# Kernel tuning notes

Measured on AMD Instinct MI355X. Metric: run time of the kernel, lower is better.

Reference implementation:

```python
import jax, jax.numpy as jnp
import numpy as np

B, N, D, H, HID = 8, 729, 1152, 12, 4304
HD = D // H
EPS = 1e-6


def _layer_norm(x, g, b):
    mu = jnp.mean(x, axis=-1, keepdims=True)
    var = jnp.mean((x - mu) ** 2, axis=-1, keepdims=True)
    return (x - mu) / jnp.sqrt(var + EPS) * g + b


def setup_inputs() -> dict:
    key = jax.random.key(0)
    ks = jax.random.split(key, 9)
    s = 0.02
    return {
        "x": jax.random.normal(ks[0], (B, N, D), jnp.float32),
        "wq": jax.random.normal(ks[1], (D, D), jnp.float32) * s,
        "bq": jnp.zeros((D,), jnp.float32),
        "wk": jax.random.normal(ks[2], (D, D), jnp.float32) * s,
        "bk": jnp.zeros((D,), jnp.float32),
        "wv": jax.random.normal(ks[3], (D, D), jnp.float32) * s,
        "bv": jnp.zeros((D,), jnp.float32),
        "wo": jax.random.normal(ks[4], (D, D), jnp.float32) * s,
        "bo": jnp.zeros((D,), jnp.float32),
        "ln1_g": jnp.ones((D,), jnp.float32),
        "ln1_b": jnp.zeros((D,), jnp.float32),
        "w_fc1": jax.random.normal(ks[5], (HID, D), jnp.float32) * s,
        "b_fc1": jnp.zeros((HID,), jnp.float32),
        "w_fc2": jax.random.normal(ks[6], (D, HID), jnp.float32) * s,
        "b_fc2": jnp.zeros((D,), jnp.float32),
        "ln2_g": jnp.ones((D,), jnp.float32),
        "ln2_b": jnp.zeros((D,), jnp.float32),
    }


def reference(x, wq, bq, wk, bk, wv, bv, wo, bo, ln1_g, ln1_b,
              w_fc1, b_fc1, w_fc2, b_fc2, ln2_g, ln2_b):
    b, n, d = x.shape
    # split_heads in the source is a plain view (B, H, N, HD) -- NOT a transpose.
    def heads(t):
        return t.reshape(b, H, n, HD)

    Q = heads(x @ wq.T + bq)
    K = heads(x @ wk.T + bk)
    V = heads(x @ wv.T + bv)

    scores = jnp.einsum("bhqd,bhkd->bhqk", Q, K) * (HD ** -0.5)
    attn_w = jax.nn.softmax(scores, axis=-1)
    o = jnp.einsum("bhqk,bhkd->bhqd", attn_w, V)  # [B,H,N,HD]
    o = jnp.swapaxes(o, 1, 2).reshape(b, n, d)
    attn_out = o @ wo.T + bo

    # post-norm: LN(sublayer) + residual
    h = _layer_norm(attn_out, ln1_g, ln1_b) + x

    # quirky MLP: activation applied BEFORE fc1 (faithful to source)
    m = jax.nn.gelu(h, approximate=True)
    m = m @ w_fc1.T + b_fc1
    m = m @ w_fc2.T + b_fc2

    return _layer_norm(m, ln2_g, ln2_b) + h
```

## Files before the change

### kernel.cpp

```cpp
#include <hip/hip_runtime.h>
#include <hip/hip_bf16.h>

#define BF16 __hip_bfloat16

typedef short short8 __attribute__((ext_vector_type(8)));
typedef short short4v __attribute__((ext_vector_type(4)));
typedef float v4f __attribute__((ext_vector_type(4)));
typedef float f4 __attribute__((ext_vector_type(4)));

__device__ float g_bp[1152];

__device__ __forceinline__ short f2bs(float f) {
    __hip_bfloat16 h = __float2bfloat16(f);
    return *(short*)&h;
}

__device__ __forceinline__ float bs2f(short s) {
    __hip_bfloat16 h = *(__hip_bfloat16*)&s;
    return __bfloat162float(h);
}

__device__ __forceinline__ void async_cp16(const BF16* g, BF16* l) {
    __builtin_amdgcn_global_load_lds(
        (const __attribute__((address_space(1))) void*)g,
        (__attribute__((address_space(3))) void*)l,
        16, 0, 0);
}

__global__ __launch_bounds__(256) void prep_kernel(
    const float* __restrict__ wq, const float* __restrict__ wk,
    const float* __restrict__ wv, const float* __restrict__ wo,
    const float* __restrict__ wfc1, const float* __restrict__ wfc2,
    const float* __restrict__ x,
    const float* __restrict__ bfc1, const float* __restrict__ bfc2,
    BF16* __restrict__ wbq, BF16* __restrict__ wbk,
    BF16* __restrict__ wbv, BF16* __restrict__ wbo,
    BF16* __restrict__ wbf1t, BF16* __restrict__ wbf2,
    BF16* __restrict__ xb)
{
    __shared__ float tile[64][65];
    const int bid = blockIdx.x;
    const int tid = threadIdx.x;

    if (bid < 16641) {
        const int i = bid * 256 + tid;
        constexpr int N_DD  = 331776;
        constexpr int N4    = 4 * N_DD;
        constexpr int N_F2  = 1253376;
        constexpr int E_F2  = N4 + N_F2;
        constexpr int N_X   = 1679616;
        constexpr int TOTAL = E_F2 + N_X;

        if (i < N4) {
            int seg = i / N_DD, j = i - seg * N_DD;
            const float* s = (seg == 0) ? wq : (seg == 1) ? wk : (seg == 2) ? wv : wo;
            BF16* d = (seg == 0) ? wbq : (seg == 1) ? wbk : (seg == 2) ? wbv : wbo;
            f4 v = ((const f4*)s)[j];
            short4v o = {f2bs(v.x), f2bs(v.y), f2bs(v.z), f2bs(v.w)};
            ((short4v*)d)[j] = o;
        } else if (i < E_F2) {
            int j = i - N4;
            int row = j / 1088;
            int c = (j - row * 1088) * 4;
            short4v o = {0, 0, 0, 0};
            if (c < 4304) {
                f4 v = *(const f4*)(wfc2 + (size_t)row * 4304 + c);
                o[0] = f2bs(v.x); o[1] = f2bs(v.y); o[2] = f2bs(v.z); o[3] = f2bs(v.w);
            }
            *(short4v*)(wbf2 + (size_t)row * 4352 + c) = o;
        } else if (i < TOTAL) {
            int j = i - E_F2;
            f4 v = ((const f4*)x)[j];
            short4v o = {f2bs(v.x), f2bs(v.y), f2bs(v.z), f2bs(v.w)};
            ((short4v*)xb)[j] = o;
        }
    } else if (bid < 17865) {
        const int b2 = bid - 16641;
        const int h0 = (b2 % 68) * 64;
        const int d0 = (b2 / 68) * 64;
#pragma unroll
        for (int i = 0; i < 4; ++i) {
            int lin = tid + i * 256;
            int r = lin >> 4, c4 = lin & 15;
            f4 v = {0.f, 0.f, 0.f, 0.f};
            if (h0 + r < 4304)
                v = *(const f4*)(wfc1 + (size_t)(h0 + r) * 1152 + d0 + c4 * 4);
            tile[r][c4 * 4 + 0] = v.x;
            tile[r][c4 * 4 + 1] = v.y;
            tile[r][c4 * 4 + 2] = v.z;
            tile[r][c4 * 4 + 3] = v.w;
        }
        __syncthreads();
#pragma unroll
        for (int i = 0; i < 2; ++i) {
            int lin = tid + i * 256;
            int dr = lin >> 3, h8 = lin & 7;
            short8 o;
#pragma unroll
            for (int e = 0; e < 8; ++e)
                o[e] = f2bs(tile[h8 * 8 + e][dr]);
            *(short8*)(wbf1t + (size_t)(d0 + dr) * 4352 + h0 + h8 * 8) = o;
        }
    } else {
        const int row = (bid - 17865) * 4 + (tid >> 6);
        const int lane = tid & 63;
        const float* wr = wfc2 + (size_t)row * 4304;
        float s = 0.f;
        for (int k = lane; k < 4304; k += 64) s += wr[k] * bfc1[k];
#pragma unroll
        for (int mm = 1; mm < 64; mm <<= 1) s += __shfl_xor(s, mm, 64);
        if (lane == 0) g_bp[row] = s + bfc2[row];
    }
}

__global__ __launch_bounds__(256) void qkv_merge_kernel(
    const BF16* __restrict__ A,
    const BF16* __restrict__ Wqkv,
    const float* __restrict__ b0, const float* __restrict__ b1,
    const float* __restrict__ b2,
    BF16* __restrict__ C, size_t cstride, int M,
    const BF16* __restrict__ W2,
    const BF16* __restrict__ W1t,
    float* __restrict__ P)
{
    __shared__ __align__(16) BF16 smem[256 * 64];
    const int bid  = blockIdx.x;
    const int tid  = threadIdx.x;
    const int lane = tid & 63;
    const int wave = tid >> 6;
    const int quad = lane >> 4;
    const int l16  = lane & 15;
    const v4f zf = {0.f, 0.f, 0.f, 0.f};

    if (bid < 324) {
        BF16* As = smem;
        BF16* Bs = smem + 64 * 64;
        const int mx = bid % 18, ny = (bid / 18) % 9, z = bid / 162;
        const int m0 = mx * 64, n0 = ny * 128;
        const int ks0 = z * 34;
        const int wm = (wave >> 1) * 32;
        const int wn = (wave & 1) * 64;

        v4f acc[2][4];
#pragma unroll
        for (int i = 0; i < 2; ++i)
#pragma unroll
            for (int j = 0; j < 4; ++j) acc[i][j] = zf;

        const BF16* gA[2]; BF16* lA[2];
#pragma unroll
        for (int i = 0; i < 2; ++i) {
            int c = tid + i * 256;
            gA[i] = W2 + (size_t)(m0 + (c >> 3)) * 4352 + ((((c & 7) - (c >> 3)) & 7) << 3)
                  + ks0 * 64;
            lA[i] = As + (c & ~63) * 8;
        }
        const BF16* gB[4]; BF16* lB[4];
#pragma unroll
        for (int i = 0; i < 4; ++i) {
            int c = tid + i * 256;
            gB[i] = W1t + (size_t)(n0 + (c >> 3)) * 4352 + ((((c & 7) - (c >> 3)) & 7) << 3)
                  + ks0 * 64;
            lB[i] = Bs + (c & ~63) * 8;
        }

        for (int kt = 0; kt < 34; ++kt) {
#pragma unroll
            for (int i = 0; i < 2; ++i) { async_cp16(gA[i], lA[i]); gA[i] += 64; }
#pragma unroll
            for (int i = 0; i < 4; ++i)  { async_cp16(gB[i], lB[i]); gB[i] += 64; }
            __syncthreads();
#pragma unroll
            for (int ks = 0; ks < 2; ++ks) {
                short8 af[2], bfg[4];
#pragma unroll
                for (int mt = 0; mt < 2; ++mt) {
                    int row = wm + mt * 16 + l16;
                    af[mt] = *(const short8*)(As + row * 64 + ((((ks << 2) | quad) + row & 7) & 7) * 8);
                }
#pragma unroll
                for (int nt = 0; nt < 4; ++nt) {
                    int row = wn + nt * 16 + l16;
                    bfg[nt] = *(const short8*)(Bs + row * 64 + ((((ks << 2) | quad) + row & 7) & 7) * 8);
                }
#pragma unroll
                for (int mt = 0; mt < 2; ++mt)
#pragma unroll
                    for (int nt = 0; nt < 4; ++nt)
                        acc[mt][nt] = __builtin_amdgcn_mfma_f32_16x16x32_bf16(
                            af[mt], bfg[nt], acc[mt][nt], 0, 0, 0);
            }
            __syncthreads();
        }

        float* Pz = P + (size_t)z * 1327104;
#pragma unroll
        for (int mt = 0; mt < 2; ++mt)
#pragma unroll
            for (int nt = 0; nt < 4; ++nt)
#pragma unroll
                for (int r2 = 0; r2 < 4; ++r2) {
                    int row = m0 + wm + mt * 16 + quad * 4 + r2;
                    int col = n0 + wn + nt * 16 + l16;
                    Pz[(size_t)row * 1152 + col] = acc[mt][nt][r2];
                }
    } else {
        BF16* As = smem;
        BF16* Bs = smem + 128 * 64;
        const int id2 = bid - 324;
        const int m0 = (id2 % 46) * 128;
        const int n0 = (id2 / 46) * 128;
        const int wm = (wave >> 1) * 64;
        const int wn = (wave & 1) * 64;

        v4f acc[4][4];
#pragma unroll
        for (int i = 0; i < 4; ++i)
#pragma unroll
            for (int j = 0; j < 4; ++j) acc[i][j] = zf;

        const BF16* gA[4]; BF16* lA[4];
        const BF16* gB[4]; BF16* lB[4];
#pragma unroll
        for (int i = 0; i < 4; ++i) {
            int c = tid + i * 256;
            int src = ((((c & 7) - (c >> 3)) & 7) << 3);
            gA[i] = A + (size_t)(m0 + (c >> 3)) * 1152 + src;
            gB[i] = Wqkv + (size_t)(n0 + (c >> 3)) * 1152 + src;
            lA[i] = As + (c & ~63) * 8;
            lB[i] = Bs + (c & ~63) * 8;
        }

        for (int kt = 0; kt < 18; ++kt) {
#pragma unroll
            for (int i = 0; i < 4; ++i) { async_cp16(gA[i], lA[i]); gA[i] += 64; }
#pragma unroll
            for (int i = 0; i < 4; ++i) { async_cp16(gB[i], lB[i]); gB[i] += 64; }
            __syncthreads();
#pragma unroll
            for (int ks = 0; ks < 2; ++ks) {
                short8 af[4], bfg[4];
#pragma unroll
                for (int mt = 0; mt < 4; ++mt) {
                    int row = wm + mt * 16 + l16;
                    af[mt] = *(const short8*)(As + row * 64 + ((((ks << 2) | quad) + row & 7) & 7) * 8);
                }
#pragma unroll
                for (int nt = 0; nt < 4; ++nt) {
                    int row = wn + nt * 16 + l16;
                    bfg[nt] = *(const short8*)(Bs + row * 64 + ((((ks << 2) | quad) + row & 7) & 7) * 8);
                }
#pragma unroll
                for (int mt = 0; mt < 4; ++mt)
#pragma unroll
                    for (int nt = 0; nt < 4; ++nt)
                        acc[mt][nt] = __builtin_amdgcn_mfma_f32_16x16x32_bf16(
                            af[mt], bfg[nt], acc[mt][nt], 0, 0, 0);
            }
            __syncthreads();
        }

        const int sel = n0 / 1152;
        const float* bp = (sel == 0) ? b0 : (sel == 1) ? b1 : b2;
        BF16* Cb = C + (size_t)sel * cstride;
        const int nl0 = n0 - sel * 1152;

        float bv[4];
#pragma unroll
        for (int nt = 0; nt < 4; ++nt)
            bv[nt] = bp[nl0 + wn + nt * 16 + l16];
#pragma unroll
        for (int mt = 0; mt < 4; ++mt)
#pragma unroll
            for (int nt = 0; nt < 4; ++nt)
#pragma unroll
                for (int r2 = 0; r2 < 4; ++r2) {
                    int row_l = wm + mt * 16 + quad * 4 + r2;
                    int col_l = wn + nt * 16 + l16;
                    smem[row_l * 128 + col_l] = __float2bfloat16(acc[mt][nt][r2] + bv[nt]);
                }
        __syncthreads();
#pragma unroll
        for (int p = 0; p < 8; ++p) {
            int idx = p * 256 + tid;
            int row = m0 + (idx >> 4);
            if (row < M)
                *(short8*)(Cb + (size_t)row * 1152 + nl0 + (idx & 15) * 8) =
                    *(const short8*)(smem + idx * 8);
        }
    }
}

__global__ __launch_bounds__(256) void trans_reduce_kernel(
    const BF16* __restrict__ V, BF16* __restrict__ VT,
    const float* __restrict__ P, BF16* __restrict__ Wm)
{
    __shared__ __align__(16) BF16 tl[64][128];
    const int bid = blockIdx.x, tid = threadIdx.x;
    const short8 zero8 = {0, 0, 0, 0, 0, 0, 0, 0};

    if (bid < 1152) {
        const int hg = bid / 12, kb = bid - hg * 12;
        const int b = hg / 12, hh = hg - b * 12;
        const BF16* src = V + (size_t)b * 839808 + (size_t)hh * 69984;
        BF16* dst = VT + (size_t)hg * 86016;
        const int kk0 = kb * 64;
#pragma unroll
        for (int i = 0; i < 3; ++i) {
            int c = tid + i * 256;
            int r = c / 12, cg = c - r * 12;
            short8 v = (kk0 + r < 729)
                ? *(const short8*)(src + (size_t)(kk0 + r) * 96 + cg * 8) : zero8;
            *(short8*)(&tl[r][(cg ^ ((r >> 3) & 7)) * 8]) = v;
        }
        __syncthreads();
#pragma unroll
        for (int i = 0; i < 3; ++i) {
            int wc = tid + i * 256;
            int hd = wc >> 3, o = wc & 7;
            int sp = (((hd >> 3) ^ o) << 3) + (hd & 7);
            short8 out;
#pragma unroll
            for (int j = 0; j < 8; ++j)
                out[j] = *(const short*)&tl[o * 8 + j][sp];
            *(short8*)(dst + (size_t)hd * 768 + kk0 + o * 8) = out;
        }
    } else if (bid < 1728) {
        int c = (bid - 1152) * 256 + tid;
        int hg = c / 1536, rem = c - hg * 1536;
        int r = rem / 96, ock = rem - r * 96;
        int kk = ock * 8;
        short8 v = zero8;
        if (r == 0) {
            const short oneb = 0x3F80;
#pragma unroll
            for (int j = 0; j < 8; ++j) v[j] = (kk + j < 729) ? oneb : (short)0;
        }
        *(short8*)(VT + (size_t)hg * 86016 + (size_t)(96 + r) * 768 + kk) = v;
    } else {
        int i = (bid - 1728) * 256 + tid;
        f4 s = ((const f4*)P)[i];
        f4 v = ((const f4*)(P + 1327104))[i];
        s.x += v.x; s.y += v.y; s.z += v.z; s.w += v.w;
        short4v o = {f2bs(s.x), f2bs(s.y), f2bs(s.z), f2bs(s.w)};
        ((short4v*)Wm)[i] = o;
    }
}

template<int TM>
__global__ __launch_bounds__(256) void gemm_bt_t(
    const BF16* __restrict__ A, int lda,
    const BF16* __restrict__ W, int ldb,
    const float* __restrict__ bias, int nbias,
    BF16* __restrict__ C, int ldc,
    int M, int Kr)
{
    constexpr int MT = TM / 32;
    __shared__ __align__(16) BF16 smem[(TM + 128) * 64];
    BF16* As = smem;
    BF16* Bs = smem + TM * 64;

    const int tid  = threadIdx.x;
    const int lane = tid & 63;
    const int wave = tid >> 6;
    const int quad = lane >> 4;
    const int l16  = lane & 15;
    const int wm   = (wave >> 1) * (TM / 2);
    const int wn   = (wave & 1) * 64;
    const int m0   = blockIdx.x * TM;
    const int n0   = blockIdx.y * 128;
    if (m0 >= M) return;

    const v4f zf = {0.f, 0.f, 0.f, 0.f};
    v4f acc[MT][4];
#pragma unroll
    for (int i = 0; i < MT; ++i)
#pragma unroll
        for (int j = 0; j < 4; ++j) acc[i][j] = zf;

    const BF16* gA[MT]; BF16* lA[MT];
#pragma unroll
    for (int i = 0; i < MT; ++i) {
        int c = tid + i * 256;
        gA[i] = A + (size_t)(m0 + (c >> 3)) * lda + ((((c & 7) - (c >> 3)) & 7) << 3);
        lA[i] = As + (c & ~63) * 8;
    }
    const BF16* gB[4]; BF16* lB[4];
#pragma unroll
    for (int i = 0; i < 4; ++i) {
        int c = tid + i * 256;
        gB[i] = W + (size_t)(n0 + (c >> 3)) * ldb + ((((c & 7) - (c >> 3)) & 7) << 3);
        lB[i] = Bs + (c & ~63) * 8;
    }

    const int nk = Kr >> 6;
    for (int kt = 0; kt < nk; ++kt) {
#pragma unroll
        for (int i = 0; i < MT; ++i) { async_cp16(gA[i], lA[i]); gA[i] += 64; }
#pragma unroll
        for (int i = 0; i < 4; ++i)  { async_cp16(gB[i], lB[i]); gB[i] += 64; }
        __syncthreads();

#pragma unroll
        for (int ks = 0; ks < 2; ++ks) {
            short8 af[MT], bfg[4];
#pragma unroll
            for (int mt = 0; mt < MT; ++mt) {
                int row = wm + mt * 16 + l16;
                af[mt] = *(const short8*)(As + row * 64 + ((((ks << 2) | quad) + row & 7) & 7) * 8);
            }
#pragma unroll
            for (int nt = 0; nt < 4; ++nt) {
                int row = wn + nt * 16 + l16;
                bfg[nt] = *(const short8*)(Bs + row * 64 + ((((ks << 2) | quad) + row & 7) & 7) * 8);
            }
#pragma unroll
            for (int mt = 0; mt < MT; ++mt)
#pragma unroll
                for (int nt = 0; nt < 4; ++nt)
                    acc[mt][nt] = __builtin_amdgcn_mfma_f32_16x16x32_bf16(
                        af[mt], bfg[nt], acc[mt][nt], 0, 0, 0);
        }
        __syncthreads();
    }

    float bv[4];
#pragma unroll
    for (int nt = 0; nt < 4; ++nt) {
        int col = n0 + wn + nt * 16 + l16;
        bv[nt] = (col < nbias) ? bias[col] : 0.f;
    }
#pragma unroll
    for (int mt = 0; mt < MT; ++mt)
#pragma unroll
        for (int nt = 0; nt < 4; ++nt)
#pragma unroll
            for (int r2 = 0; r2 < 4; ++r2) {
                int row_l = wm + mt * 16 + quad * 4 + r2;
                int col_l = wn + nt * 16 + l16;
                smem[row_l * 128 + col_l] = __float2bfloat16(acc[mt][nt][r2] + bv[nt]);
            }
    __syncthreads();
#pragma unroll
    for (int p = 0; p < TM / 16; ++p) {
        int idx = p * 256 + tid;
        int row = m0 + (idx >> 4);
        if (row < M)
            *(short8*)(C + (size_t)row * ldc + n0 + (idx & 15) * 8) =
                *(const short8*)(smem + idx * 8);
    }
}

__global__ __launch_bounds__(256) void attn_flash3(
    const BF16* __restrict__ Q, const BF16* __restrict__ K,
    const BF16* __restrict__ VT, BF16* __restrict__ O)
{
    constexpr int NQ = 729, HDk = 96, DM = 1152, LDV = 768;
    __shared__ __align__(16) BF16 Ks[64 * 104];
    __shared__ __align__(16) BF16 Vs[112 * 64];
    __shared__ __align__(16) BF16 Ps[4][32 * 72];

    const int id = blockIdx.x;
    const int xcd = id & 7, slot = id >> 3;
    const int hb = slot / 6, qt = slot - hb * 6;
    const int hg = xcd * 12 + hb;
    const int b = hg / 12, hh = hg - b * 12;

    const int tid = threadIdx.x, wave = tid >> 6, lane = tid & 63;
    const int quad = lane >> 4, l16 = lane & 15;
    const size_t kbase = (size_t)b * (NQ * DM) + (size_t)hh * (NQ * HDk);
    const size_t vbase = (size_t)hg * 112 * LDV;

    const short8 zero8 = {0, 0, 0, 0, 0, 0, 0, 0};
    const v4f zf = {0.f, 0.f, 0.f, 0.f};
    const float C2 = 0.14724445f;

    const int q0w = qt * 128 + wave * 32;
    short8 aq[2][3];
#pragma unroll
    for (int mt = 0; mt < 2; ++mt) {
        int qrow = q0w + mt * 16 + l16;
#pragma unroll
        for (int ks = 0; ks < 3; ++ks)
            aq[mt][ks] = (qrow < NQ)
                ? *(const short8*)(Q + kbase + (size_t)qrow * HDk + ks * 32 + quad * 8)
                : zero8;
    }

    int kk_[3], kg_[3];
#pragma unroll
    for (int i = 0; i < 3; ++i) {
        int c = tid + i * 256;
        kk_[i] = c / 12; kg_[i] = c - kk_[i] * 12;
    }
    int vq_[4], vgr_[4], vhd_[4];
#pragma unroll
    for (int i = 0; i < 4; ++i) {
        int q = wave + 4 * i;
        vq_[i] = q;
        int hd = q * 8 + (lane >> 3);
        vhd_[i] = hd;
        vgr_[i] = ((lane & 7) - hd) & 7;
    }

    v4f oacc[2][7];
#pragma unroll
    for (int mt = 0; mt < 2; ++mt)
#pragma unroll
        for (int nt = 0; nt < 7; ++nt) oacc[mt][nt] = zf;

    for (int kt = 0; kt < 12; ++kt) {
        const int k0 = kt * 64;
#pragma unroll
        for (int i = 0; i < 4; ++i) {
            if (vq_[i] < 14)
                async_cp16(VT + vbase + (size_t)vhd_[i] * LDV + k0 + vgr_[i] * 8,
                           Vs + vq_[i] * 512);
        }
#pragma unroll
        for (int i = 0; i < 3; ++i) {
            short8 v = *(const short8*)(K + kbase + (size_t)(k0 + kk_[i]) * HDk + kg_[i] * 8);
            *(short8*)(Ks + kk_[i] * 104 + kg_[i] * 8) = v;
        }
        __syncthreads();

        v4f s[2][4];
#pragma unroll
        for (int mt = 0; mt < 2; ++mt)
#pragma unroll
            for (int nt = 0; nt < 4; ++nt) s[mt][nt] = zf;
#pragma unroll
        for (int ks = 0; ks < 3; ++ks)
#pragma unroll
            for (int nt = 0; nt < 4; ++nt) {
                short8 bk = *(const short8*)(Ks + (nt * 16 + l16) * 104 + ks * 32 + quad * 8);
#pragma unroll
                for (int mt = 0; mt < 2; ++mt)
                    s[mt][nt] = __builtin_amdgcn_mfma_f32_16x16x32_bf16(
                        aq[mt][ks], bk, s[mt][nt], 0, 0, 0);
            }

        BF16* Pw = &Ps[wave][0];
#pragma unroll
        for (int mt = 0; mt < 2; ++mt)
#pragma unroll
            for (int nt = 0; nt < 4; ++nt)
#pragma unroll
                for (int r = 0; r < 4; ++r)
                    Pw[(mt * 16 + quad * 4 + r) * 72 + nt * 16 + l16] =
                        __float2bfloat16(exp2f(s[mt][nt][r] * C2));
        asm volatile("s_waitcnt lgkmcnt(0)" ::: "memory");

        short8 ap[2][2];
#pragma unroll
        for (int mt = 0; mt < 2; ++mt)
#pragma unroll
            for (int kc = 0; kc < 2; ++kc)
                ap[mt][kc] = *(const short8*)(Pw + (mt * 16 + l16) * 72 + kc * 32 + quad * 8);
#pragma unroll
        for (int nt = 0; nt < 7; ++nt) {
            int hd = nt * 16 + l16;
#pragma unroll
            for (int kc = 0; kc < 2; ++kc) {
                short8 bv = *(const short8*)(Vs + hd * 64 + (((kc * 4 + quad) + hd & 7) & 7) * 8);
#pragma unroll
                for (int mt = 0; mt < 2; ++mt)
                    oacc[mt][nt] = __builtin_amdgcn_mfma_f32_16x16x32_bf16(
                        ap[mt][kc], bv, oacc[mt][nt], 0, 0, 0);
            }
        }
        __syncthreads();
    }

#pragma unroll
    for (int mt = 0; mt < 2; ++mt) {
        const int qb = q0w + mt * 16 + quad * 4;
#pragma unroll
        for (int r = 0; r < 4; ++r) {
            int q = qb + r;
            float lv = __shfl(oacc[mt][6][r], quad << 4, 64);
            float inv = (lv > 0.f) ? 1.f / lv : 0.f;
            if (q >= NQ) continue;
#pragma unroll
            for (int nt = 0; nt < 6; ++nt)
                O[(size_t)b * (NQ * DM) + (size_t)q * DM + hh * HDk + nt * 16 + l16] =
                    __float2bfloat16(oacc[mt][nt][r] * inv);
        }
    }
}

__device__ __forceinline__ float block_sum256(float v, float* red, int tid)
{
#pragma unroll
    for (int mm = 1; mm < 64; mm <<= 1) v += __shfl_xor(v, mm, 64);
    if ((tid & 63) == 0) red[tid >> 6] = v;
    __syncthreads();
    float r = red[0] + red[1] + red[2] + red[3];
    __syncthreads();
    return r;
}

__global__ __launch_bounds__(256) void ln1_gelu_kernel(
    const BF16* __restrict__ ao, const float* __restrict__ x,
    const float* __restrict__ gw, const float* __restrict__ bw,
    BF16* __restrict__ hout, BF16* __restrict__ gout)
{
    __shared__ float red[4];
    const int row = blockIdx.x, tid = threadIdx.x;
    const bool act = tid < 144;
    float v[8];
    float s = 0.f;
    if (act) {
        short8 pk = ((const short8*)(ao + (size_t)row * 1152))[tid];
#pragma unroll
        for (int j = 0; j < 8; ++j) { v[j] = bs2f(pk[j]); s += v[j]; }
    } else {
#pragma unroll
        for (int j = 0; j < 8; ++j) v[j] = 0.f;
    }
    s = block_sum256(s, red, tid);
    float mu = s * (1.f / 1152.f);
    float vsum = 0.f;
    if (act) {
#pragma unroll
        for (int j = 0; j < 8; ++j) { float d = v[j] - mu; vsum += d * d; }
    }
    vsum = block_sum256(vsum, red, tid);
    float rstd = rsqrtf(vsum * (1.f / 1152.f) + 1e-6f);
    if (act) {
        f4 g0 = ((const f4*)gw)[2 * tid], g1 = ((const f4*)gw)[2 * tid + 1];
        f4 b0 = ((const f4*)bw)[2 * tid], b1 = ((const f4*)bw)[2 * tid + 1];
        const f4* xr = (const f4*)(x + (size_t)row * 1152);
        f4 x0 = xr[2 * tid], x1 = xr[2 * tid + 1];
        short8 ho, go;
#pragma unroll
        for (int j = 0; j < 8; ++j) {
            float gj = (j < 4) ? g0[j] : g1[j - 4];
            float bj = (j < 4) ? b0[j] : b1[j - 4];
            float xj = (j < 4) ? x0[j] : x1[j - 4];
            float hv = (v[j] - mu) * rstd * gj + bj + xj;
            ho[j] = f2bs(hv);
            float t = hv;
            float gl = 0.5f * t * (1.f + tanhf(0.7978845608028654f * (t + 0.044715f * t * t * t)));
            go[j] = f2bs(gl);
        }
        ((short8*)(hout + (size_t)row * 1152))[tid] = ho;
        ((short8*)(gout + (size_t)row * 1152))[tid] = go;
    }
}

__global__ __launch_bounds__(256) void ln2_kernel(
    const BF16* __restrict__ m2, const BF16* __restrict__ hf,
    const float* __restrict__ gw, const float* __restrict__ bw,
    float* __restrict__ out)
{
    __shared__ float red[4];
    const int row = blockIdx.x, tid = threadIdx.x;
    const bool act = tid < 144;
    float v[8];
    float s = 0.f;
    if (act) {
        short8 pk = ((const short8*)(m2 + (size_t)row * 1152))[tid];
#pragma unroll
        for (int j = 0; j < 8; ++j) { v[j] = bs2f(pk[j]); s += v[j]; }
    } else {
#pragma unroll
        for (int j = 0; j < 8; ++j) v[j] = 0.f;
    }
    s = block_sum256(s, red, tid);
    float mu = s * (1.f / 1152.f);
    float vsum = 0.f;
    if (act) {
#pragma unroll
        for (int j = 0; j < 8; ++j) { float d = v[j] - mu; vsum += d * d; }
    }
    vsum = block_sum256(vsum, red, tid);
    float rstd = rsqrtf(vsum * (1.f / 1152.f) + 1e-6f);
    if (act) {
        f4 g0 = ((const f4*)gw)[2 * tid], g1 = ((const f4*)gw)[2 * tid + 1];
        f4 b0 = ((const f4*)bw)[2 * tid], b1 = ((const f4*)bw)[2 * tid + 1];
        short8 hfv = ((const short8*)(hf + (size_t)row * 1152))[tid];
        f4 o0, o1;
#pragma unroll
        for (int j = 0; j < 8; ++j) {
            float gj = (j < 4) ? g0[j] : g1[j - 4];
            float bj = (j < 4) ? b0[j] : b1[j - 4];
            float ov = (v[j] - mu) * rstd * gj + bj + bs2f(hfv[j]);
            if (j < 4) o0[j] = ov; else o1[j - 4] = ov;
        }
        f4* orow = (f4*)(out + (size_t)row * 1152);
        orow[2 * tid] = o0;
        orow[2 * tid + 1] = o1;
    }
}

extern "C" void kernel_launch(void* const* d_in, const int* in_sizes, int n_in,
                              void* d_out, int out_size, void* d_ws, size_t ws_size,
                              hipStream_t stream)
{
    const float* x    = (const float*)d_in[0];
    const float* wq   = (const float*)d_in[1];
    const float* bq   = (const float*)d_in[2];
    const float* wk   = (const float*)d_in[3];
    const float* bk   = (const float*)d_in[4];
    const float* wv   = (const float*)d_in[5];
    const float* bv   = (const float*)d_in[6];
    const float* wo   = (const float*)d_in[7];
    const float* bo   = (const float*)d_in[8];
    const float* ln1g = (const float*)d_in[9];
    const float* ln1b = (const float*)d_in[10];
    const float* wfc1 = (const float*)d_in[11];
    const float* bfc1 = (const float*)d_in[12];
    const float* wfc2 = (const float*)d_in[13];
    const float* bfc2 = (const float*)d_in[14];
    const float* ln2g = (const float*)d_in[15];
    const float* ln2b = (const float*)d_in[16];

    const int T = 8 * 729;
    const int D = 1152, HIDP = 4352;
    const size_t TD = (size_t)T * D;
    const size_t WDD = (size_t)D * D;

    BF16* wbq   = (BF16*)d_ws;
    BF16* wbk   = wbq + WDD;
    BF16* wbv   = wbk + WDD;
    BF16* wbo   = wbv + WDD;
    BF16* wbf1t = wbo + WDD;
    BF16* wbf2  = wbf1t + (size_t)HIDP * D;
    BF16* xb    = wbf2 + (size_t)D * HIDP;
    BF16* S0    = xb + TD;
    BF16* S1    = S0 + TD;
    BF16* S2    = S1 + TD;
    BF16* S3    = S2 + TD;
    BF16* C0    = S3 + TD;
    BF16* C1    = C0 + TD;
    BF16* VT    = C0;
    float* Pws  = (float*)S3;
    BF16* Wm    = xb;

    static float* bp_dev = nullptr;
    if (!bp_dev) hipGetSymbolAddress((void**)&bp_dev, HIP_SYMBOL(g_bp));

    dim3 blk(256);

    prep_kernel<<<18153, blk, 0, stream>>>(
        wq, wk, wv, wo, wfc1, wfc2, x, bfc1, bfc2,
        wbq, wbk, wbv, wbo, wbf1t, wbf2, xb);

    qkv_merge_kernel<<<1566, blk, 0, stream>>>(
        xb, wbq, bq, bk, bv, S0, TD, T, wbf2, wbf1t, Pws);

    trans_reduce_kernel<<<3024, blk, 0, stream>>>(S2, VT, Pws, Wm);

    attn_flash3<<<576, blk, 0, stream>>>(S0, S1, VT, S3);

    gemm_bt_t<64><<<dim3(92, 9), blk, 0, stream>>>(S3, D, wbo, D, bo, D, C0, D, T, D);

    ln1_gelu_kernel<<<T, blk, 0, stream>>>(C0, x, ln1g, ln1b, C1, C0);

    gemm_bt_t<64><<<dim3(92, 9), blk, 0, stream>>>(C0, D, Wm, D, bp_dev, D, S3, D, T, D);

    ln2_kernel<<<T, blk, 0, stream>>>(S3, C1, ln2g, ln2b, (float*)d_out);
}
```

Baseline: 401.6 us.

## Drop split-K fp32 partials for merged MLP weight; swizzle attention P tile

The merged fc2·fc1 weight product was computed as a 2-way split-K GEMM that wrote fp32 partials, then reduced and converted to bf16 in the transpose kernel. It is now computed as full-K 128x128 tiles that write bf16 straight into a global device buffer. This removes the partial-buffer traffic and the reduce pass. In exchange, 81 long-running blocks share the launch with the QKV tiles, which may leave a scheduling tail. Separately, the attention kernel's per-wave P staging buffer drops its row padding in favour of an XOR swizzle, to avoid LDS bank conflicts with less shared memory.

```diff
diff --git a/kernel.cpp b/kernel.cpp
--- a/kernel.cpp
+++ b/kernel.cpp
@@ -9,6 +9,7 @@
 typedef float f4 __attribute__((ext_vector_type(4)));
 
 __device__ float g_bp[1152];
+__device__ BF16  g_wm[1152 * 1152];
 
 __device__ __forceinline__ short f2bs(float f) {
     __hip_bfloat16 h = __float2bfloat16(f);
@@ -113,15 +114,14 @@
     }
 }
 
-__global__ __launch_bounds__(256) void qkv_merge_kernel(
+__global__ __launch_bounds__(256) void qkv_wm_kernel(
     const BF16* __restrict__ A,
     const BF16* __restrict__ Wqkv,
     const float* __restrict__ b0, const float* __restrict__ b1,
     const float* __restrict__ b2,
     BF16* __restrict__ C, size_t cstride, int M,
     const BF16* __restrict__ W2,
-    const BF16* __restrict__ W1t,
-    float* __restrict__ P)
+    const BF16* __restrict__ W1t)
 {
     __shared__ __align__(16) BF16 smem[256 * 64];
     const int bid  = blockIdx.x;
@@ -130,51 +130,45 @@
     const int wave = tid >> 6;
     const int quad = lane >> 4;
     const int l16  = lane & 15;
+    const int wm   = (wave >> 1) * 64;
+    const int wn   = (wave & 1) * 64;
     const v4f zf = {0.f, 0.f, 0.f, 0.f};
-
-    if (bid < 324) {
-        BF16* As = smem;
-        BF16* Bs = smem + 64 * 64;
-        const int mx = bid % 18, ny = (bid / 18) % 9, z = bid / 162;
-        const int m0 = mx * 64, n0 = ny * 128;
-        const int ks0 = z * 34;
-        const int wm = (wave >> 1) * 32;
-        const int wn = (wave & 1) * 64;
-
-        v4f acc[2][4];
-#pragma unroll
-        for (int i = 0; i < 2; ++i)
-#pragma unroll
-            for (int j = 0; j < 4; ++j) acc[i][j] = zf;
-
-        const BF16* gA[2]; BF16* lA[2];
-#pragma unroll
-        for (int i = 0; i < 2; ++i) {
-            int c = tid + i * 256;
-            gA[i] = W2 + (size_t)(m0 + (c >> 3)) * 4352 + ((((c & 7) - (c >> 3)) & 7) << 3)
-                  + ks0 * 64;
-            lA[i] = As + (c & ~63) * 8;
-        }
+    BF16* As = smem;
+    BF16* Bs = smem + 128 * 64;
+
+    v4f acc[4][4];
+#pragma unroll
+    for (int i = 0; i < 4; ++i)
+#pragma unroll
+        for (int j = 0; j < 4; ++j) acc[i][j] = zf;
+
+    if (bid < 81) {
+        const int m0 = (bid % 9) * 128;
+        const int n0 = (bid / 9) * 128;
+
+        const BF16* gA[4]; BF16* lA[4];
         const BF16* gB[4]; BF16* lB[4];
 #pragma unroll
         for (int i = 0; i < 4; ++i) {
             int c = tid + i * 256;
-            gB[i] = W1t + (size_t)(n0 + (c >> 3)) * 4352 + ((((c & 7) - (c >> 3)) & 7) << 3)
-                  + ks0 * 64;
+            int src = ((((c & 7) - (c >> 3)) & 7) << 3);
+            gA[i] = W2 + (size_t)(m0 + (c >> 3)) * 4352 + src;
+            gB[i] = W1t + (size_t)(n0 + (c >> 3)) * 4352 + src;
+            lA[i] = As + (c & ~63) * 8;
             lB[i] = Bs + (c & ~63) * 8;
         }
 
-        for (int kt = 0; kt < 34; ++kt) {
-#pragma unroll
-            for (int i = 0; i < 2; ++i) { async_cp16(gA[i], lA[i]); gA[i] += 64; }
-#pragma unroll
-            for (int i = 0; i < 4; ++i)  { async_cp16(gB[i], lB[i]); gB[i] += 64; }
+        for (int kt = 0; kt < 68; ++kt) {
+#pragma unroll
+            for (int i = 0; i < 4; ++i) { async_cp16(gA[i], lA[i]); gA[i] += 64; }
+#pragma unroll
+            for (int i = 0; i < 4; ++i) { async_cp16(gB[i], lB[i]); gB[i] += 64; }
             __syncthreads();
 #pragma unroll
             for (int ks = 0; ks < 2; ++ks) {
-                short8 af[2], bfg[4];
-#pragma unroll
-                for (int mt = 0; mt < 2; ++mt) {
+                short8 af[4], bfg[4];
+#pragma unroll
+                for (int mt = 0; mt < 4; ++mt) {
                     int row = wm + mt * 16 + l16;
                     af[mt] = *(const short8*)(As + row * 64 + ((((ks << 2) | quad) + row & 7) & 7) * 8);
                 }
@@ -184,7 +178,7 @@
                     bfg[nt] = *(const short8*)(Bs + row * 64 + ((((ks << 2) | quad) + row & 7) & 7) * 8);
                 }
 #pragma unroll
-                for (int mt = 0; mt < 2; ++mt)
+                for (int mt = 0; mt < 4; ++mt)
 #pragma unroll
                     for (int nt = 0; nt < 4; ++nt)
                         acc[mt][nt] = __builtin_amdgcn_mfma_f32_16x16x32_bf16(
@@ -193,31 +187,27 @@
             __syncthreads();
         }
 
-        float* Pz = P + (size_t)z * 1327104;
-#pragma unroll
-        for (int mt = 0; mt < 2; ++mt)
+#pragma unroll
+        for (int mt = 0; mt < 4; ++mt)
 #pragma unroll
             for (int nt = 0; nt < 4; ++nt)
 #pragma unroll
                 for (int r2 = 0; r2 < 4; ++r2) {
-                    int row = m0 + wm + mt * 16 + quad * 4 + r2;
-                    int col = n0 + wn + nt * 16 + l16;
-                    Pz[(size_t)row * 1152 + col] = acc[mt][nt][r2];
+                    int row_l = wm + mt * 16 + quad * 4 + r2;
+                    int col_l = wn + nt * 16 + l16;
+                    smem[row_l * 128 + col_l] = __float2bfloat16(acc[mt][nt][r2]);
                 }
+        __syncthreads();
+#pragma unroll
+        for (int p = 0; p < 8; ++p) {
+            int idx = p * 256 + tid;
+            *(short8*)(g_wm + (size_t)(m0 + (idx >> 4)) * 1152 + n0 + (idx & 15) * 8) =
+                *(const short8*)(smem + idx * 8);
+        }
     } else {
-        BF16* As = smem;
-        BF16* Bs = smem + 128 * 64;
-        const int id2 = bid - 324;
+        const int id2 = bid - 81;
         const int m0 = (id2 % 46) * 128;
         const int n0 = (id2 / 46) * 128;
-        const int wm = (wave >> 1) * 64;
-        const int wn = (wave & 1) * 64;
-
-        v4f acc[4][4];
-#pragma unroll
-        for (int i = 0; i < 4; ++i)
-#pragma unroll
-            for (int j = 0; j < 4; ++j) acc[i][j] = zf;
 
         const BF16* gA[4]; BF16* lA[4];
         const BF16* gB[4]; BF16* lB[4];
@@ -291,9 +281,8 @@
     }
 }
 
-__global__ __launch_bounds__(256) void trans_reduce_kernel(
-    const BF16* __restrict__ V, BF16* __restrict__ VT,
-    const float* __restrict__ P, BF16* __restrict__ Wm)
+__global__ __launch_bounds__(256) void trans_kernel(
+    const BF16* __restrict__ V, BF16* __restrict__ VT)
 {
     __shared__ __align__(16) BF16 tl[64][128];
     const int bid = blockIdx.x, tid = threadIdx.x;
@@ -325,7 +314,7 @@
                 out[j] = *(const short*)&tl[o * 8 + j][sp];
             *(short8*)(dst + (size_t)hd * 768 + kk0 + o * 8) = out;
         }
-    } else if (bid < 1728) {
+    } else {
         int c = (bid - 1152) * 256 + tid;
         int hg = c / 1536, rem = c - hg * 1536;
         int r = rem / 96, ock = rem - r * 96;
@@ -337,13 +326,6 @@
             for (int j = 0; j < 8; ++j) v[j] = (kk + j < 729) ? oneb : (short)0;
         }
         *(short8*)(VT + (size_t)hg * 86016 + (size_t)(96 + r) * 768 + kk) = v;
-    } else {
-        int i = (bid - 1728) * 256 + tid;
-        f4 s = ((const f4*)P)[i];
-        f4 v = ((const f4*)(P + 1327104))[i];
-        s.x += v.x; s.y += v.y; s.z += v.z; s.w += v.w;
-        short4v o = {f2bs(s.x), f2bs(s.y), f2bs(s.z), f2bs(s.w)};
-        ((short4v*)Wm)[i] = o;
     }
 }
 
@@ -458,7 +440,7 @@
     constexpr int NQ = 729, HDk = 96, DM = 1152, LDV = 768;
     __shared__ __align__(16) BF16 Ks[64 * 104];
     __shared__ __align__(16) BF16 Vs[112 * 64];
-    __shared__ __align__(16) BF16 Ps[4][32 * 72];
+    __shared__ __align__(16) BF16 Ps[4][32 * 64];
 
     const int id = blockIdx.x;
     const int xcd = id & 7, slot = id >> 3;
@@ -547,7 +529,9 @@
             for (int nt = 0; nt < 4; ++nt)
 #pragma unroll
                 for (int r = 0; r < 4; ++r)
-                    Pw[(mt * 16 + quad * 4 + r) * 72 + nt * 16 + l16] =
+                    Pw[((mt * 16 + quad * 4 + r) << 6)
+                       + ((((nt << 1) | (l16 >> 3)) ^ (quad << 1)) << 3)
+                       + (l16 & 7)] =
                         __float2bfloat16(exp2f(s[mt][nt][r] * C2));
         asm volatile("s_waitcnt lgkmcnt(0)" ::: "memory");
 
@@ -556,7 +540,8 @@
         for (int mt = 0; mt < 2; ++mt)
 #pragma unroll
             for (int kc = 0; kc < 2; ++kc)
-                ap[mt][kc] = *(const short8*)(Pw + (mt * 16 + l16) * 72 + kc * 32 + quad * 8);
+                ap[mt][kc] = *(const short8*)(Pw + ((mt * 16 + l16) << 6)
+                    + ((((kc << 2) | quad) ^ (((l16 >> 2) & 3) << 1)) << 3));
 #pragma unroll
         for (int nt = 0; nt < 7; ++nt) {
             int hd = nt * 16 + l16;
@@ -735,11 +720,11 @@
     BF16* C0    = S3 + TD;
     BF16* C1    = C0 + TD;
     BF16* VT    = C0;
-    float* Pws  = (float*)S3;
-    BF16* Wm    = xb;
 
     static float* bp_dev = nullptr;
+    static BF16*  wm_dev = nullptr;
     if (!bp_dev) hipGetSymbolAddress((void**)&bp_dev, HIP_SYMBOL(g_bp));
+    if (!wm_dev) hipGetSymbolAddress((void**)&wm_dev, HIP_SYMBOL(g_wm));
 
     dim3 blk(256);
 
@@ -747,10 +732,10 @@
         wq, wk, wv, wo, wfc1, wfc2, x, bfc1, bfc2,
         wbq, wbk, wbv, wbo, wbf1t, wbf2, xb);
 
-    qkv_merge_kernel<<<1566, blk, 0, stream>>>(
-        xb, wbq, bq, bk, bv, S0, TD, T, wbf2, wbf1t, Pws);
-
-    trans_reduce_kernel<<<3024, blk, 0, stream>>>(S2, VT, Pws, Wm);
+    qkv_wm_kernel<<<1323, blk, 0, stream>>>(
+        xb, wbq, bq, bk, bv, S0, TD, T, wbf2, wbf1t);
+
+    trans_kernel<<<1728, blk, 0, stream>>>(S2, VT);
 
     attn_flash3<<<576, blk, 0, stream>>>(S0, S1, VT, S3);
 
@@ -758,7 +743,7 @@
 
     ln1_gelu_kernel<<<T, blk, 0, stream>>>(C0, x, ln1g, ln1b, C1, C0);
 
-    gemm_bt_t<64><<<dim3(92, 9), blk, 0, stream>>>(C0, D, Wm, D, bp_dev, D, S3, D, T, D);
+    gemm_bt_t<64><<<dim3(92, 9), blk, 0, stream>>>(C0, D, wm_dev, D, bp_dev, D, S3, D, T, D);
 
     ln2_kernel<<<T, blk, 0, stream>>>(S3, C1, ln2g, ln2b, (float*)d_out);
 }
```

New measurement: 397.1 us. Within noise of the previous version (-1.1%).
